# Performance work log

Measured on AMD Instinct MI355X. Metric: run time of the kernel, lower is better.

The kernel has to match this reference:

```python
import jax, jax.numpy as jnp
import numpy as np

B, S, D = 2, 2048, 1024
HEADS, HEAD_DIM = 16, 64

def setup_inputs() -> dict:
    key = jax.random.key(0)
    ks = jax.random.split(key, 5)
    sc = 0.02
    return {
        "hidden_states": jax.random.normal(ks[0], (B, S, D), jnp.float32),
        "Wq": jax.random.normal(ks[1], (D, HEADS * HEAD_DIM), jnp.float32) * sc,
        "Wk": jax.random.normal(ks[2], (D, HEADS * HEAD_DIM), jnp.float32) * sc,
        "Wv": jax.random.normal(ks[3], (D, HEADS * HEAD_DIM), jnp.float32) * sc,
        "Wo": jax.random.normal(ks[4], (HEADS * HEAD_DIM, D), jnp.float32) * sc,
        "bo": jnp.zeros((D,), jnp.float32),
    }

def reference(hidden_states, Wq, Wk, Wv, Wo, bo):
    b, s, _ = hidden_states.shape
    # QKV projections (no bias, as in diffusers Attention defaults)
    q = (hidden_states @ Wq).reshape(b, s, HEADS, HEAD_DIM).transpose(0, 2, 1, 3)
    k = (hidden_states @ Wk).reshape(b, s, HEADS, HEAD_DIM).transpose(0, 2, 1, 3)
    v = (hidden_states @ Wv).reshape(b, s, HEADS, HEAD_DIM).transpose(0, 2, 1, 3)
    scale = 1.0 / jnp.sqrt(jnp.asarray(HEAD_DIM, hidden_states.dtype))
    scores = jnp.einsum('bhqd,bhkd->bhqk', q, k) * scale  # full NxN scores
    attn = jax.nn.softmax(scores, axis=-1)
    out = jnp.einsum('bhqk,bhkd->bhqd', attn, v)
    out = out.transpose(0, 2, 1, 3).reshape(b, s, HEADS * HEAD_DIM)
    return out @ Wo + bo
```

## Files before the change

### kernel.cpp

```cpp
#include <hip/hip_runtime.h>

#define B_ 2
#define S_ 2048
#define D_ 1024
#define H_ 16
#define HD_ 64
#define M_ (B_ * S_)

typedef __attribute__((ext_vector_type(4))) float f32x4;
typedef __attribute__((ext_vector_type(16))) float f32x16;
typedef __attribute__((ext_vector_type(8))) short s16x8;
typedef unsigned short u16;
typedef unsigned int u32;

#define QSCALE 0.1803368801111204f

__device__ __forceinline__ u16 f2bf(float f) {
  unsigned u = __float_as_uint(f);
  u += 0x7fffu + ((u >> 16) & 1u);
  return (u16)(u >> 16);
}

__device__ __forceinline__ u32 cvtpk_bf16(float lo, float hi) {
  u32 r;
  asm("v_cvt_pk_bf16_f32 %0, %1, %2" : "=v"(r) : "v"(lo), "v"(hi));
  return r;
}

__device__ __forceinline__ void g2lds16(const u16* g, u16* l) {
  __builtin_amdgcn_global_load_lds((const __attribute__((address_space(1))) u32*)(g),
                                   (__attribute__((address_space(3))) u32*)(l), 16, 0, 0);
}

__global__ __launch_bounds__(256) void prep_kernel(
    const float* __restrict__ X, const float* __restrict__ Wq,
    const float* __restrict__ Wk, const float* __restrict__ Wv,
    const float* __restrict__ Wo, u16* __restrict__ Xb, u16* __restrict__ Wt0) {
  __shared__ float tile[32][33];
  const int id = blockIdx.x;
  if (id < 2048) {
    int i = (id * 256 + threadIdx.x) * 8;
    const float4 va = *(const float4*)(X + i);
    const float4 vb = *(const float4*)(X + i + 4);
    union { u32 u[4]; s16x8 v; } pk;
    pk.u[0] = cvtpk_bf16(va.x, va.y); pk.u[1] = cvtpk_bf16(va.z, va.w);
    pk.u[2] = cvtpk_bf16(vb.x, vb.y); pk.u[3] = cvtpk_bf16(vb.z, vb.w);
    *(s16x8*)(Xb + i) = pk.v;
    return;
  }
  const int id2 = id - 2048;
  const int z = id2 >> 10;
  const float* W = (z == 0) ? Wq : (z == 1) ? Wk : (z == 2) ? Wv : Wo;
  u16* Wt = Wt0 + (size_t)z * (D_ * D_);
  const float sc = (z == 0) ? QSCALE : 1.0f;
  const int tx = threadIdx.x & 31, ty = threadIdx.x >> 5;
  const int c0 = (id2 & 31) * 32, r0 = ((id2 >> 5) & 31) * 32;
#pragma unroll
  for (int j = 0; j < 32; j += 8)
    tile[ty + j][tx] = W[(size_t)(r0 + ty + j) * D_ + c0 + tx];
  __syncthreads();
#pragma unroll
  for (int j = 0; j < 32; j += 8)
    Wt[(size_t)(c0 + ty + j) * D_ + r0 + tx] = f2bf(tile[tx][ty + j] * sc);
}

__global__ __launch_bounds__(256) void gemm_qkv_kernel(
    const u16* __restrict__ Xb, const u16* __restrict__ WqT,
    const u16* __restrict__ WkT, const u16* __restrict__ WvT,
    u16* __restrict__ Qb, u16* __restrict__ Kb, u16* __restrict__ Vt) {
  __shared__ u16 ldsraw[16384];
  u16 (*As)[4096] = (u16(*)[4096])ldsraw;
  u16 (*Bs)[4096] = (u16(*)[4096])(ldsraw + 8192);
  const int tid = threadIdx.x;
  const int lane = tid & 63, wid = tid >> 6;
  const int wr = wid >> 1, wc = wid & 1;
  const int l15 = lane & 15, l4 = lane >> 4;
  const int bm = blockIdx.x * 128;
  const int bn128 = blockIdx.y;
  const int sel = bn128 >> 3;
  const u16* Wt = (sel == 0) ? WqT : (sel == 1) ? WkT : WvT;
  const int bn = (bn128 & 7) * 128;
  const int r0 = lane >> 2;
  const int c0 = lane & 3;

#define GSTAGE(buf, kt)                                                          \
  do {                                                                           \
    _Pragma("unroll") for (int j = 0; j < 2; ++j) {                              \
      const int row = (wid * 2 + j) * 16 + r0;                                   \
      g2lds16(Xb + (size_t)(bm + row) * D_ + (kt) + c0 * 8,                      \
              &As[buf][(wid * 2 + j) * 512]);                                    \
      g2lds16(Wt + (size_t)(bn + row) * D_ + (kt) + c0 * 8,                      \
              &Bs[buf][(wid * 2 + j) * 512]);                                    \
    }                                                                            \
  } while (0)

  f32x4 acc[4][4] = {};
  GSTAGE(0, 0);
  __syncthreads();
  int cur = 0;
  for (int kt = 0; kt < D_; kt += 32) {
    GSTAGE(cur ^ 1, (kt + 32) & (D_ - 1));
    s16x8 af[4], bfr[4];
#pragma unroll
    for (int i = 0; i < 4; ++i) af[i] = *(const s16x8*)&As[cur][(wr * 64 + i * 16 + l15) * 32 + l4 * 8];
#pragma unroll
    for (int j = 0; j < 4; ++j) bfr[j] = *(const s16x8*)&Bs[cur][(wc * 64 + j * 16 + l15) * 32 + l4 * 8];
#pragma unroll
    for (int i = 0; i < 4; ++i)
#pragma unroll
      for (int j = 0; j < 4; ++j)
        acc[i][j] = __builtin_amdgcn_mfma_f32_16x16x32_bf16(af[i], bfr[j], acc[i][j], 0, 0, 0);
    __syncthreads();
    cur ^= 1;
  }
#undef GSTAGE

  const int bb = bm >> 11, sb = bm & (S_ - 1);
  u16* T = ldsraw;

  if (sel == 2) {
#pragma unroll
    for (int i = 0; i < 4; ++i)
#pragma unroll
      for (int j = 0; j < 4; ++j) {
        const int n = wc * 64 + j * 16 + l15;
        const int mcol = wr * 64 + i * 16 + l4 * 4;
        ushort4 v;
        v.x = f2bf(acc[i][j][0]); v.y = f2bf(acc[i][j][1]);
        v.z = f2bf(acc[i][j][2]); v.w = f2bf(acc[i][j][3]);
        const u32 off = (u32)((n * 128 + mcol) * 2) ^ (u32)((n & 7) << 4);
        *(ushort4*)((char*)T + off) = v;
      }
    __syncthreads();
#pragma unroll
    for (int p = 0; p < 8; ++p) {
      const int c = p * 256 + tid;
      const int drow = c >> 4, k = c & 15;
      const int h = (bn + drow) >> 6, d = (bn + drow) & 63;
      const u32 off = (u32)((drow * 128 + k * 8) * 2) ^ (u32)((drow & 7) << 4);
      *(s16x8*)(Vt + ((size_t)(bb * H_ + h) * HD_ + d) * S_ + sb + k * 8) =
          *(const s16x8*)((const char*)T + off);
    }
  } else {
#pragma unroll
    for (int i = 0; i < 4; ++i)
#pragma unroll
      for (int j = 0; j < 4; ++j)
#pragma unroll
        for (int r = 0; r < 4; ++r) {
          const int m = wr * 64 + i * 16 + l4 * 4 + r;
          const int n = wc * 64 + j * 16 + l15;
          const u32 off = (u32)((m * 128 + n) * 2) ^ (u32)((m & 7) << 4);
          *(u16*)((char*)T + off) = f2bf(acc[i][j][r]);
        }
    __syncthreads();
    u16* dst = (sel == 0) ? Qb : Kb;
#pragma unroll
    for (int p = 0; p < 8; ++p) {
      const int c = p * 256 + tid;
      const int hh = c >> 10;
      const int cc = c & 1023;
      const int srow = cc >> 3, k = cc & 7;
      const int h = (bn >> 6) + hh;
      const u32 off = (u32)((srow * 128 + hh * 64 + k * 8) * 2) ^ (u32)((srow & 7) << 4);
      *(s16x8*)(dst + ((size_t)(bb * H_ + h) * S_ + sb + srow) * HD_ + k * 8) =
          *(const s16x8*)((const char*)T + off);
    }
  }
}

__global__ __launch_bounds__(512, 2) void attn_kernel(
    const u16* __restrict__ Qb, const u16* __restrict__ Kb,
    const u16* __restrict__ Vt, u16* __restrict__ Ob) {
  __shared__ char smem_raw[65536];
  typedef u16 (*lds_t)[2][4096];
  lds_t Ks = (lds_t)smem_raw;
  lds_t Vs = (lds_t)(smem_raw + 32768);
  const int tid = threadIdx.x;
  const int lane = tid & 63, wid = tid >> 6;
  const int qg = wid & 3, half = wid >> 2;
  const int l31 = lane & 31, hi = lane >> 5;
  const int id = blockIdx.x;
  const int bh = (id & 7) * 4 + (id >> 6);
  const int qx = (id >> 3) & 7;
  const size_t kbase = (size_t)bh * S_ * HD_;
  const size_t vbase = (size_t)bh * HD_ * S_;
  const int q0 = qx * 256 + qg * 64;
  const int r0 = lane >> 3;
  const int cs = ((lane & 7) ^ r0) * 8;
  const int kv0 = half << 10;

#define STAGE(buf, kvv)                                                          \
  do {                                                                           \
    _Pragma("unroll") for (int j = 0; j < 2; ++j) {                              \
      const int row = (qg * 2 + j) * 8 + r0;                                     \
      g2lds16(Kb + kbase + (size_t)((kvv) + row) * HD_ + cs,                     \
              &Ks[half][buf][(qg * 2 + j) * 512]);                               \
      g2lds16(Vt + vbase + (size_t)row * S_ + (kvv) + cs,                        \
              &Vs[half][buf][(qg * 2 + j) * 512]);                               \
    }                                                                            \
  } while (0)

  STAGE(0, kv0);

  s16x8 aqA[4], aqB[4];
#pragma unroll
  for (int kc = 0; kc < 4; ++kc) {
    aqA[kc] = *(const s16x8*)(Qb + kbase + (size_t)(q0 + l31) * HD_ + kc * 16 + hi * 8);
    aqB[kc] = *(const s16x8*)(Qb + kbase + (size_t)(q0 + 32 + l31) * HD_ + kc * 16 + hi * 8);
  }

  const short one_bf = (short)0x3F80;
  const s16x8 ones8 = {one_bf, one_bf, one_bf, one_bf, one_bf, one_bf, one_bf, one_bf};

  f32x16 accA0 = {}, accA1 = {}, accB0 = {}, accB1 = {};
  f32x16 lsaccA = {}, lsaccB = {};

  int choff[4];
#pragma unroll
  for (int c = 0; c < 4; ++c) choff[c] = ((c * 2 + hi) ^ (l31 & 7)) * 8;

  __syncthreads();

  for (int t = 0; t < 16; ++t) {
    const int buf = t & 1;
    STAGE(buf ^ 1, kv0 + (((t + 1) & 15) << 6));

    f32x16 sA0 = {}, sA1 = {}, sB0 = {}, sB1 = {};
    __builtin_amdgcn_s_setprio(1);
#pragma unroll
    for (int kc = 0; kc < 4; ++kc) {
      const s16x8 ka0 = *(const s16x8*)&Ks[half][buf][(l31) * 64 + choff[kc]];
      const s16x8 ka1 = *(const s16x8*)&Ks[half][buf][(32 + l31) * 64 + choff[kc]];
      sA0 = __builtin_amdgcn_mfma_f32_32x32x16_bf16(ka0, aqA[kc], sA0, 0, 0, 0);
      sB0 = __builtin_amdgcn_mfma_f32_32x32x16_bf16(ka0, aqB[kc], sB0, 0, 0, 0);
      sA1 = __builtin_amdgcn_mfma_f32_32x32x16_bf16(ka1, aqA[kc], sA1, 0, 0, 0);
      sB1 = __builtin_amdgcn_mfma_f32_32x32x16_bf16(ka1, aqB[kc], sB1, 0, 0, 0);
    }
    __builtin_amdgcn_s_setprio(0);

#pragma unroll
    for (int r = 0; r < 16; ++r) {
      sA0[r] = __builtin_amdgcn_exp2f(sA0[r]);
      sA1[r] = __builtin_amdgcn_exp2f(sA1[r]);
      sB0[r] = __builtin_amdgcn_exp2f(sB0[r]);
      sB1[r] = __builtin_amdgcn_exp2f(sB1[r]);
    }

    s16x8 paA[4], paB[4];
#pragma unroll
    for (int c = 0; c < 4; ++c) {
      const int rr = (c & 1) * 8;
      u32 a0, a1, b0, b1;
      if (c < 2) {
        a0 = cvtpk_bf16(sA0[rr + 0], sA0[rr + 1]);
        a1 = cvtpk_bf16(sA0[rr + 2], sA0[rr + 3]);
        b0 = cvtpk_bf16(sA0[rr + 4], sA0[rr + 5]);
        b1 = cvtpk_bf16(sA0[rr + 6], sA0[rr + 7]);
      } else {
        a0 = cvtpk_bf16(sA1[rr + 0], sA1[rr + 1]);
        a1 = cvtpk_bf16(sA1[rr + 2], sA1[rr + 3]);
        b0 = cvtpk_bf16(sA1[rr + 4], sA1[rr + 5]);
        b1 = cvtpk_bf16(sA1[rr + 6], sA1[rr + 7]);
      }
      asm volatile("v_permlane32_swap_b32 %0, %1" : "+v"(a0), "+v"(b0));
      asm volatile("v_permlane32_swap_b32 %0, %1" : "+v"(a1), "+v"(b1));
      union { u32 u[4]; s16x8 v; } pk;
      pk.u[0] = a0; pk.u[1] = a1; pk.u[2] = b0; pk.u[3] = b1;
      paA[c] = pk.v;
    }
#pragma unroll
    for (int c = 0; c < 4; ++c) {
      const int rr = (c & 1) * 8;
      u32 a0, a1, b0, b1;
      if (c < 2) {
        a0 = cvtpk_bf16(sB0[rr + 0], sB0[rr + 1]);
        a1 = cvtpk_bf16(sB0[rr + 2], sB0[rr + 3]);
        b0 = cvtpk_bf16(sB0[rr + 4], sB0[rr + 5]);
        b1 = cvtpk_bf16(sB0[rr + 6], sB0[rr + 7]);
      } else {
        a0 = cvtpk_bf16(sB1[rr + 0], sB1[rr + 1]);
        a1 = cvtpk_bf16(sB1[rr + 2], sB1[rr + 3]);
        b0 = cvtpk_bf16(sB1[rr + 4], sB1[rr + 5]);
        b1 = cvtpk_bf16(sB1[rr + 6], sB1[rr + 7]);
      }
      asm volatile("v_permlane32_swap_b32 %0, %1" : "+v"(a0), "+v"(b0));
      asm volatile("v_permlane32_swap_b32 %0, %1" : "+v"(a1), "+v"(b1));
      union { u32 u[4]; s16x8 v; } pk;
      pk.u[0] = a0; pk.u[1] = a1; pk.u[2] = b0; pk.u[3] = b1;
      paB[c] = pk.v;
    }

    __builtin_amdgcn_s_setprio(1);
#pragma unroll
    for (int c = 0; c < 4; ++c) {
      const s16x8 vb0 = *(const s16x8*)&Vs[half][buf][(l31) * 64 + choff[c]];
      const s16x8 vb1 = *(const s16x8*)&Vs[half][buf][(32 + l31) * 64 + choff[c]];
      accA0 = __builtin_amdgcn_mfma_f32_32x32x16_bf16(paA[c], vb0, accA0, 0, 0, 0);
      accB0 = __builtin_amdgcn_mfma_f32_32x32x16_bf16(paB[c], vb0, accB0, 0, 0, 0);
      accA1 = __builtin_amdgcn_mfma_f32_32x32x16_bf16(paA[c], vb1, accA1, 0, 0, 0);
      accB1 = __builtin_amdgcn_mfma_f32_32x32x16_bf16(paB[c], vb1, accB1, 0, 0, 0);
      lsaccA = __builtin_amdgcn_mfma_f32_32x32x16_bf16(paA[c], ones8, lsaccA, 0, 0, 0);
      lsaccB = __builtin_amdgcn_mfma_f32_32x32x16_bf16(paB[c], ones8, lsaccB, 0, 0, 0);
    }
    __builtin_amdgcn_s_setprio(0);

    __syncthreads();
  }
#undef STAGE

  const int bb = bh >> 4, h = bh & 15;
  float (*MB)[64][49] = (float(*)[64][49])smem_raw;

  if (half) {
#pragma unroll
    for (int r = 0; r < 16; ++r) {
      MB[qg][lane][r] = accA0[r];
      MB[qg][lane][16 + r] = accA1[r];
      MB[qg][lane][32 + r] = lsaccA[r];
    }
  }
  __syncthreads();
  if (!half) {
#pragma unroll
    for (int r = 0; r < 16; ++r) {
      const float o0 = accA0[r] + MB[qg][lane][r];
      const float o1 = accA1[r] + MB[qg][lane][16 + r];
      const float rinv = 1.0f / (lsaccA[r] + MB[qg][lane][32 + r]);
      const int qrow = (r & 3) + 8 * (r >> 2) + 4 * hi;
      const int q = q0 + qrow;
      Ob[(size_t)(bb * S_ + q) * (H_ * HD_) + h * HD_ + l31] = f2bf(o0 * rinv);
      Ob[(size_t)(bb * S_ + q) * (H_ * HD_) + h * HD_ + 32 + l31] = f2bf(o1 * rinv);
    }
  }
  __syncthreads();
  if (half) {
#pragma unroll
    for (int r = 0; r < 16; ++r) {
      MB[qg][lane][r] = accB0[r];
      MB[qg][lane][16 + r] = accB1[r];
      MB[qg][lane][32 + r] = lsaccB[r];
    }
  }
  __syncthreads();
  if (!half) {
#pragma unroll
    for (int r = 0; r < 16; ++r) {
      const float o0 = accB0[r] + MB[qg][lane][r];
      const float o1 = accB1[r] + MB[qg][lane][16 + r];
      const float rinv = 1.0f / (lsaccB[r] + MB[qg][lane][32 + r]);
      const int qrow = (r & 3) + 8 * (r >> 2) + 4 * hi;
      const int q = q0 + 32 + qrow;
      Ob[(size_t)(bb * S_ + q) * (H_ * HD_) + h * HD_ + l31] = f2bf(o0 * rinv);
      Ob[(size_t)(bb * S_ + q) * (H_ * HD_) + h * HD_ + 32 + l31] = f2bf(o1 * rinv);
    }
  }
}

__global__ __launch_bounds__(256, 2) void gemm_o_kernel(
    const u16* __restrict__ A, const u16* __restrict__ Bt,
    const float* __restrict__ bias, float* __restrict__ C) {
  __shared__ u16 As[2][128 * 32];
  __shared__ u16 Bs[2][64 * 32];
  const int tid = threadIdx.x;
  const int lane = tid & 63, wid = tid >> 6;
  const int l15 = lane & 15, l4 = lane >> 4;
  const int bm = blockIdx.x * 128;
  const int bn = blockIdx.y * 64;
  const int r0 = lane >> 2;
  const int c0 = lane & 3;

#define GSTAGE(buf, kt)                                                          \
  do {                                                                           \
    _Pragma("unroll") for (int j = 0; j < 2; ++j) {                              \
      const int row = (wid * 2 + j) * 16 + r0;                                   \
      g2lds16(A + (size_t)(bm + row) * D_ + (kt) + c0 * 8,                       \
              &As[buf][(wid * 2 + j) * 512]);                                    \
    }                                                                            \
    g2lds16(Bt + (size_t)(bn + wid * 16 + r0) * D_ + (kt) + c0 * 8,              \
            &Bs[buf][wid * 512]);                                                \
  } while (0)

  f32x4 acc[2][4] = {};
  GSTAGE(0, 0);
  __syncthreads();
  int cur = 0;
  for (int kt = 0; kt < D_; kt += 32) {
    GSTAGE(cur ^ 1, (kt + 32) & (D_ - 1));
    s16x8 af[2], bfr[4];
#pragma unroll
    for (int i = 0; i < 2; ++i) af[i] = *(const s16x8*)&As[cur][(wid * 32 + i * 16 + l15) * 32 + l4 * 8];
#pragma unroll
    for (int j = 0; j < 4; ++j) bfr[j] = *(const s16x8*)&Bs[cur][(j * 16 + l15) * 32 + l4 * 8];
#pragma unroll
    for (int i = 0; i < 2; ++i)
#pragma unroll
      for (int j = 0; j < 4; ++j)
        acc[i][j] = __builtin_amdgcn_mfma_f32_16x16x32_bf16(af[i], bfr[j], acc[i][j], 0, 0, 0);
    __syncthreads();
    cur ^= 1;
  }
#undef GSTAGE
#pragma unroll
  for (int i = 0; i < 2; ++i)
#pragma unroll
    for (int j = 0; j < 4; ++j)
#pragma unroll
      for (int r = 0; r < 4; ++r) {
        int m = bm + wid * 32 + i * 16 + l4 * 4 + r;
        int n = bn + j * 16 + l15;
        C[(size_t)m * D_ + n] = acc[i][j][r] + bias[n];
      }
}

extern "C" void kernel_launch(void* const* d_in, const int* in_sizes, int n_in,
                              void* d_out, int out_size, void* d_ws, size_t ws_size,
                              hipStream_t stream) {
  const float* X  = (const float*)d_in[0];
  const float* Wq = (const float*)d_in[1];
  const float* Wk = (const float*)d_in[2];
  const float* Wv = (const float*)d_in[3];
  const float* Wo = (const float*)d_in[4];
  const float* bo = (const float*)d_in[5];
  float* out = (float*)d_out;

  char* w = (char*)d_ws;
  u16* Xb  = (u16*)(w);
  u16* WT  = (u16*)(w + (8u << 20));
  u16* WqT = WT;
  u16* WkT = WT + (1u << 20);
  u16* WvT = WT + (2u << 20);
  u16* WoT = WT + (3u << 20);
  u16* Qb  = (u16*)(w + (16u << 20));
  u16* Kb  = (u16*)(w + (24u << 20));
  u16* Vt  = (u16*)(w + (32u << 20));
  u16* Ob  = (u16*)(w + (40u << 20));

  prep_kernel<<<6144, 256, 0, stream>>>(X, Wq, Wk, Wv, Wo, Xb, WT);
  gemm_qkv_kernel<<<dim3(32, 24), 256, 0, stream>>>(Xb, WqT, WkT, WvT, Qb, Kb, Vt);
  attn_kernel<<<256, 512, 0, stream>>>(Qb, Kb, Vt, Ob);
  gemm_o_kernel<<<dim3(32, 16), 256, 0, stream>>>(Ob, WoT, bo, out);
}
```

Before: 109.2 us.

## Quad-buffer K/V in LDS and interleave two KV tiles' QK^T with PV

Grows LDS to 128 KB with four K/V stage buffers and processes two 64-wide KV tiles per loop iteration, with one barrier per pair instead of per tile. The second tile's QK^T MFMAs are issued before the first tile's PV MFMAs so matrix work can overlap the exp/pack VALU phase. The larger LDS footprint and the removed occupancy hint in launch bounds likely limit the kernel to one 512-thread block per CU. Register pressure also rises because two score sets are live at once.

Measured after the change: 138.2 us. 1.27x slower.

```diff
diff --git a/kernel.cpp b/kernel.cpp
--- a/kernel.cpp
+++ b/kernel.cpp
@@ -169,13 +169,13 @@
   }
 }
 
-__global__ __launch_bounds__(512, 2) void attn_kernel(
+__global__ __launch_bounds__(512) void attn_kernel(
     const u16* __restrict__ Qb, const u16* __restrict__ Kb,
     const u16* __restrict__ Vt, u16* __restrict__ Ob) {
-  __shared__ char smem_raw[65536];
-  typedef u16 (*lds_t)[2][4096];
+  __shared__ char smem_raw[131072];
+  typedef u16 (*lds_t)[4][4096];
   lds_t Ks = (lds_t)smem_raw;
-  lds_t Vs = (lds_t)(smem_raw + 32768);
+  lds_t Vs = (lds_t)(smem_raw + 65536);
   const int tid = threadIdx.x;
   const int lane = tid & 63, wid = tid >> 6;
   const int qg = wid & 3, half = wid >> 2;
@@ -201,7 +201,88 @@
     }                                                                            \
   } while (0)
 
+#define QKT(S0A, S1A, S0B, S1B, BUF)                                             \
+  do {                                                                           \
+    __builtin_amdgcn_s_setprio(1);                                               \
+    _Pragma("unroll") for (int kc = 0; kc < 4; ++kc) {                           \
+      const s16x8 ka0 = *(const s16x8*)&Ks[half][BUF][(l31) * 64 + choff[kc]];   \
+      const s16x8 ka1 = *(const s16x8*)&Ks[half][BUF][(32 + l31) * 64 + choff[kc]]; \
+      S0A = __builtin_amdgcn_mfma_f32_32x32x16_bf16(ka0, aqA[kc], S0A, 0, 0, 0); \
+      S0B = __builtin_amdgcn_mfma_f32_32x32x16_bf16(ka0, aqB[kc], S0B, 0, 0, 0); \
+      S1A = __builtin_amdgcn_mfma_f32_32x32x16_bf16(ka1, aqA[kc], S1A, 0, 0, 0); \
+      S1B = __builtin_amdgcn_mfma_f32_32x32x16_bf16(ka1, aqB[kc], S1B, 0, 0, 0); \
+    }                                                                            \
+    __builtin_amdgcn_s_setprio(0);                                               \
+  } while (0)
+
+#define EXPPACK(S0A, S1A, S0B, S1B, PA, PB)                                      \
+  do {                                                                           \
+    _Pragma("unroll") for (int r = 0; r < 16; ++r) {                             \
+      S0A[r] = __builtin_amdgcn_exp2f(S0A[r]);                                   \
+      S1A[r] = __builtin_amdgcn_exp2f(S1A[r]);                                   \
+      S0B[r] = __builtin_amdgcn_exp2f(S0B[r]);                                   \
+      S1B[r] = __builtin_amdgcn_exp2f(S1B[r]);                                   \
+    }                                                                            \
+    _Pragma("unroll") for (int c = 0; c < 4; ++c) {                              \
+      const int rr = (c & 1) * 8;                                                \
+      u32 a0, a1, b0, b1;                                                        \
+      if (c < 2) {                                                               \
+        a0 = cvtpk_bf16(S0A[rr + 0], S0A[rr + 1]);                               \
+        a1 = cvtpk_bf16(S0A[rr + 2], S0A[rr + 3]);                               \
+        b0 = cvtpk_bf16(S0A[rr + 4], S0A[rr + 5]);                               \
+        b1 = cvtpk_bf16(S0A[rr + 6], S0A[rr + 7]);                               \
+      } else {                                                                   \
+        a0 = cvtpk_bf16(S1A[rr + 0], S1A[rr + 1]);                               \
+        a1 = cvtpk_bf16(S1A[rr + 2], S1A[rr + 3]);                               \
+        b0 = cvtpk_bf16(S1A[rr + 4], S1A[rr + 5]);                               \
+        b1 = cvtpk_bf16(S1A[rr + 6], S1A[rr + 7]);                               \
+      }                                                                          \
+      asm volatile("v_permlane32_swap_b32 %0, %1" : "+v"(a0), "+v"(b0));         \
+      asm volatile("v_permlane32_swap_b32 %0, %1" : "+v"(a1), "+v"(b1));         \
+      union { u32 u[4]; s16x8 v; } pk;                                           \
+      pk.u[0] = a0; pk.u[1] = a1; pk.u[2] = b0; pk.u[3] = b1;                    \
+      PA[c] = pk.v;                                                              \
+    }                                                                            \
+    _Pragma("unroll") for (int c = 0; c < 4; ++c) {                              \
+      const int rr = (c & 1) * 8;                                                \
+      u32 a0, a1, b0, b1;                                                        \
+      if (c < 2) {                                                               \
+        a0 = cvtpk_bf16(S0B[rr + 0], S0B[rr + 1]);                               \
+        a1 = cvtpk_bf16(S0B[rr + 2], S0B[rr + 3]);                               \
+        b0 = cvtpk_bf16(S0B[rr + 4], S0B[rr + 5]);                               \
+        b1 = cvtpk_bf16(S0B[rr + 6], S0B[rr + 7]);                               \
+      } else {                                                                   \
+        a0 = cvtpk_bf16(S1B[rr + 0], S1B[rr + 1]);                               \
+        a1 = cvtpk_bf16(S1B[rr + 2], S1B[rr + 3]);                               \
+        b0 = cvtpk_bf16(S1B[rr + 4], S1B[rr + 5]);                               \
+        b1 = cvtpk_bf16(S1B[rr + 6], S1B[rr + 7]);                               \
+      }                                                                          \
+      asm volatile("v_permlane32_swap_b32 %0, %1" : "+v"(a0), "+v"(b0));         \
+      asm volatile("v_permlane32_swap_b32 %0, %1" : "+v"(a1), "+v"(b1));         \
+      union { u32 u[4]; s16x8 v; } pk;                                           \
+      pk.u[0] = a0; pk.u[1] = a1; pk.u[2] = b0; pk.u[3] = b1;                    \
+      PB[c] = pk.v;                                                              \
+    }                                                                            \
+  } while (0)
+
+#define PVX(PA, PB, BUF)                                                         \
+  do {                                                                           \
+    __builtin_amdgcn_s_setprio(1);                                               \
+    _Pragma("unroll") for (int c = 0; c < 4; ++c) {                              \
+      const s16x8 vb0 = *(const s16x8*)&Vs[half][BUF][(l31) * 64 + choff[c]];    \
+      const s16x8 vb1 = *(const s16x8*)&Vs[half][BUF][(32 + l31) * 64 + choff[c]]; \
+      accA0 = __builtin_amdgcn_mfma_f32_32x32x16_bf16(PA[c], vb0, accA0, 0, 0, 0); \
+      accB0 = __builtin_amdgcn_mfma_f32_32x32x16_bf16(PB[c], vb0, accB0, 0, 0, 0); \
+      accA1 = __builtin_amdgcn_mfma_f32_32x32x16_bf16(PA[c], vb1, accA1, 0, 0, 0); \
+      accB1 = __builtin_amdgcn_mfma_f32_32x32x16_bf16(PB[c], vb1, accB1, 0, 0, 0); \
+      lsaccA = __builtin_amdgcn_mfma_f32_32x32x16_bf16(PA[c], ones8, lsaccA, 0, 0, 0); \
+      lsaccB = __builtin_amdgcn_mfma_f32_32x32x16_bf16(PB[c], ones8, lsaccB, 0, 0, 0); \
+    }                                                                            \
+    __builtin_amdgcn_s_setprio(0);                                               \
+  } while (0)
+
   STAGE(0, kv0);
+  STAGE(1, kv0 + 64);
 
   s16x8 aqA[4], aqB[4];
 #pragma unroll
@@ -222,92 +303,31 @@
 
   __syncthreads();
 
-  for (int t = 0; t < 16; ++t) {
-    const int buf = t & 1;
-    STAGE(buf ^ 1, kv0 + (((t + 1) & 15) << 6));
+#pragma unroll 1
+  for (int i = 0; i < 8; ++i) {
+    const int ba = (2 * i) & 3, bbf = (2 * i + 1) & 3;
+    STAGE((2 * i + 2) & 3, kv0 + (((2 * i + 2) & 15) << 6));
+    STAGE((2 * i + 3) & 3, kv0 + (((2 * i + 3) & 15) << 6));
 
     f32x16 sA0 = {}, sA1 = {}, sB0 = {}, sB1 = {};
-    __builtin_amdgcn_s_setprio(1);
-#pragma unroll
-    for (int kc = 0; kc < 4; ++kc) {
-      const s16x8 ka0 = *(const s16x8*)&Ks[half][buf][(l31) * 64 + choff[kc]];
-      const s16x8 ka1 = *(const s16x8*)&Ks[half][buf][(32 + l31) * 64 + choff[kc]];
-      sA0 = __builtin_amdgcn_mfma_f32_32x32x16_bf16(ka0, aqA[kc], sA0, 0, 0, 0);
-      sB0 = __builtin_amdgcn_mfma_f32_32x32x16_bf16(ka0, aqB[kc], sB0, 0, 0, 0);
-      sA1 = __builtin_amdgcn_mfma_f32_32x32x16_bf16(ka1, aqA[kc], sA1, 0, 0, 0);
-      sB1 = __builtin_amdgcn_mfma_f32_32x32x16_bf16(ka1, aqB[kc], sB1, 0, 0, 0);
-    }
-    __builtin_amdgcn_s_setprio(0);
-
-#pragma unroll
-    for (int r = 0; r < 16; ++r) {
-      sA0[r] = __builtin_amdgcn_exp2f(sA0[r]);
-      sA1[r] = __builtin_amdgcn_exp2f(sA1[r]);
-      sB0[r] = __builtin_amdgcn_exp2f(sB0[r]);
-      sB1[r] = __builtin_amdgcn_exp2f(sB1[r]);
-    }
-
-    s16x8 paA[4], paB[4];
-#pragma unroll
-    for (int c = 0; c < 4; ++c) {
-      const int rr = (c & 1) * 8;
-      u32 a0, a1, b0, b1;
-      if (c < 2) {
-        a0 = cvtpk_bf16(sA0[rr + 0], sA0[rr + 1]);
-        a1 = cvtpk_bf16(sA0[rr + 2], sA0[rr + 3]);
-        b0 = cvtpk_bf16(sA0[rr + 4], sA0[rr + 5]);
-        b1 = cvtpk_bf16(sA0[rr + 6], sA0[rr + 7]);
-      } else {
-        a0 = cvtpk_bf16(sA1[rr + 0], sA1[rr + 1]);
-        a1 = cvtpk_bf16(sA1[rr + 2], sA1[rr + 3]);
-        b0 = cvtpk_bf16(sA1[rr + 4], sA1[rr + 5]);
-        b1 = cvtpk_bf16(sA1[rr + 6], sA1[rr + 7]);
-      }
-      asm volatile("v_permlane32_swap_b32 %0, %1" : "+v"(a0), "+v"(b0));
-      asm volatile("v_permlane32_swap_b32 %0, %1" : "+v"(a1), "+v"(b1));
-      union { u32 u[4]; s16x8 v; } pk;
-      pk.u[0] = a0; pk.u[1] = a1; pk.u[2] = b0; pk.u[3] = b1;
-      paA[c] = pk.v;
-    }
-#pragma unroll
-    for (int c = 0; c < 4; ++c) {
-      const int rr = (c & 1) * 8;
-      u32 a0, a1, b0, b1;
-      if (c < 2) {
-        a0 = cvtpk_bf16(sB0[rr + 0], sB0[rr + 1]);
-        a1 = cvtpk_bf16(sB0[rr + 2], sB0[rr + 3]);
-        b0 = cvtpk_bf16(sB0[rr + 4], sB0[rr + 5]);
-        b1 = cvtpk_bf16(sB0[rr + 6], sB0[rr + 7]);
-      } else {
-        a0 = cvtpk_bf16(sB1[rr + 0], sB1[rr + 1]);
-        a1 = cvtpk_bf16(sB1[rr + 2], sB1[rr + 3]);
-        b0 = cvtpk_bf16(sB1[rr + 4], sB1[rr + 5]);
-        b1 = cvtpk_bf16(sB1[rr + 6], sB1[rr + 7]);
-      }
-      asm volatile("v_permlane32_swap_b32 %0, %1" : "+v"(a0), "+v"(b0));
-      asm volatile("v_permlane32_swap_b32 %0, %1" : "+v"(a1), "+v"(b1));
-      union { u32 u[4]; s16x8 v; } pk;
-      pk.u[0] = a0; pk.u[1] = a1; pk.u[2] = b0; pk.u[3] = b1;
-      paB[c] = pk.v;
-    }
-
-    __builtin_amdgcn_s_setprio(1);
-#pragma unroll
-    for (int c = 0; c < 4; ++c) {
-      const s16x8 vb0 = *(const s16x8*)&Vs[half][buf][(l31) * 64 + choff[c]];
-      const s16x8 vb1 = *(const s16x8*)&Vs[half][buf][(32 + l31) * 64 + choff[c]];
-      accA0 = __builtin_amdgcn_mfma_f32_32x32x16_bf16(paA[c], vb0, accA0, 0, 0, 0);
-      accB0 = __builtin_amdgcn_mfma_f32_32x32x16_bf16(paB[c], vb0, accB0, 0, 0, 0);
-      accA1 = __builtin_amdgcn_mfma_f32_32x32x16_bf16(paA[c], vb1, accA1, 0, 0, 0);
-      accB1 = __builtin_amdgcn_mfma_f32_32x32x16_bf16(paB[c], vb1, accB1, 0, 0, 0);
-      lsaccA = __builtin_amdgcn_mfma_f32_32x32x16_bf16(paA[c], ones8, lsaccA, 0, 0, 0);
-      lsaccB = __builtin_amdgcn_mfma_f32_32x32x16_bf16(paB[c], ones8, lsaccB, 0, 0, 0);
-    }
-    __builtin_amdgcn_s_setprio(0);
+    QKT(sA0, sA1, sB0, sB1, ba);
+    s16x8 paAa[4], paBa[4];
+    EXPPACK(sA0, sA1, sB0, sB1, paAa, paBa);
+
+    f32x16 tA0 = {}, tA1 = {}, tB0 = {}, tB1 = {};
+    QKT(tA0, tA1, tB0, tB1, bbf);
+    PVX(paAa, paBa, ba);
+
+    s16x8 paAb[4], paBb[4];
+    EXPPACK(tA0, tA1, tB0, tB1, paAb, paBb);
+    PVX(paAb, paBb, bbf);
 
     __syncthreads();
   }
 #undef STAGE
+#undef QKT
+#undef EXPPACK
+#undef PVX
 
   const int bb = bh >> 4, h = bh & 15;
   float (*MB)[64][49] = (float(*)[64][49])smem_raw;
```
